# Performance work log

Hardware: AMD Instinct MI355X
Metric: run time of the kernel (lower is better)

## Reference

```python
import jax, jax.numpy as jnp
import numpy as np

N_NODES = 100000


def _gcn_layer(h, W, b, src, dst, norm, n):
    # h: [N, Fin] -> transform then normalized scatter-add aggregation
    h = h @ W                                   # [N, Fout]
    msg = h[src] * norm[:, None]                # [E', Fout] gather + scale
    out = jax.ops.segment_sum(msg, dst, num_segments=n)  # scatter-add
    return out + b


def setup_inputs() -> dict:
    key = jax.random.key(0)
    k1, k2, k3, k4 = jax.random.split(key, 4)
    N, F_IN, HID, C, E = N_NODES, 512, 128, 40, 1600000
    x = jax.random.normal(k1, (N, F_IN), dtype=jnp.float32)
    edge_index = jax.random.randint(k2, (2, E), 0, N, dtype=jnp.int64)
    W1 = jax.random.normal(k3, (F_IN, HID), dtype=jnp.float32) * (1.0 / np.sqrt(F_IN))
    b1 = jnp.zeros((HID,), dtype=jnp.float32)
    W2 = jax.random.normal(k4, (HID, C), dtype=jnp.float32) * (1.0 / np.sqrt(HID))
    b2 = jnp.zeros((C,), dtype=jnp.float32)
    return {"x": x, "edge_index": edge_index, "W1": W1, "b1": b1, "W2": W2, "b2": b2}


def reference(x, edge_index, W1, b1, W2, b2):
    n = x.shape[0]
    # add self-loops (GCNConv default)
    loop = jnp.arange(n, dtype=edge_index.dtype)
    src = jnp.concatenate([edge_index[0], loop])
    dst = jnp.concatenate([edge_index[1], loop])
    # symmetric normalization: deg counted on destination (in-degree, incl. self-loop)
    deg = jax.ops.segment_sum(jnp.ones_like(dst, dtype=x.dtype), dst, num_segments=n)
    dis = jnp.where(deg > 0, jax.lax.rsqrt(deg), 0.0)  # deg^{-1/2}
    norm = dis[src] * dis[dst]                          # per-edge weight

    h = jax.nn.relu(_gcn_layer(x, W1, b1, src, dst, norm, n))
    # dropout: identity in eval mode (training=False)
    h = _gcn_layer(h, W2, b2, src, dst, norm, n)
    return jax.nn.log_softmax(h, axis=1)
```

## Files before the change

### kernel.cpp

```cpp
#include <hip/hip_runtime.h>
#include <hip/hip_bf16.h>


#define F_IN 512
#define HID  128
#define NC   40
#define NCP  48

typedef __attribute__((ext_vector_type(8))) short bf16x8;
typedef __attribute__((ext_vector_type(4))) float f32x4v;

__device__ __forceinline__ ushort f2bf(float f) {
    unsigned r;
    asm("v_cvt_pk_bf16_f32 %0, %1, %1" : "=v"(r) : "v"(f));
    return (ushort)r;
}
__device__ __forceinline__ unsigned cvtpk(float a, float b) {
    unsigned r;
    asm("v_cvt_pk_bf16_f32 %0, %1, %2" : "=v"(r) : "v"(a), "v"(b));
    return r;
}
__device__ __forceinline__ float bf2f(ushort u) {
    return __uint_as_float((unsigned)u << 16);
}
__device__ __forceinline__ bf16x8 cvt8(float4 lo, float4 hi) {
    union { unsigned u[4]; bf16x8 v; } t;
    t.u[0] = cvtpk(lo.x, lo.y); t.u[1] = cvtpk(lo.z, lo.w);
    t.u[2] = cvtpk(hi.x, hi.y); t.u[3] = cvtpk(hi.z, hi.w);
    return t.v;
}

__global__ void prep_k(const int* __restrict__ dst, int E, int EB,
                       unsigned* __restrict__ cnt, int* __restrict__ rank,
                       const float* __restrict__ W1, const float* __restrict__ W2,
                       ushort* __restrict__ W1p, ushort* __restrict__ W2p) {
    int b = blockIdx.x;
    if (b < EB) {
        int t = b * 256 + threadIdx.x;
        if (t < E) rank[t] = (int)atomicAdd(&cnt[dst[t]], 1u);
        return;
    }
    int t = (b - EB) * 256 + threadIdx.x;
    if (t < 65536) {
        int j = t & 7, n = (t >> 3) & 127, kb = (t >> 10) & 3, s = t >> 12;
        int k = s * 32 + kb * 8 + j;
        W1p[t] = f2bf(W1[(size_t)k * HID + n]);
    } else {
        int q = t - 65536;
        if (q < 6144) {
            int j = q & 7;
            int i2 = q >> 3;
            int n = i2 % 48;
            int i3 = i2 / 48;
            int kb = i3 & 3, ks = i3 >> 2;
            int k = ks * 32 + kb * 8 + j;
            float v = (n < NC) ? W2[(size_t)k * NC + n] : 0.f;
            W2p[q] = f2bf(v);
        }
    }
}

__global__ __launch_bounds__(1024) void scan_block(const unsigned* __restrict__ cnt,
                                                   unsigned* __restrict__ offs,
                                                   unsigned* __restrict__ bsums,
                                                   float* __restrict__ dis, int N) {
    int tid = threadIdx.x;
    int i = blockIdx.x * 1024 + tid;
    unsigned v = (i < N) ? cnt[i] : 0u;
    if (i < N) dis[i] = rsqrtf((float)v + 1.0f);
    int lane = tid & 63, w = tid >> 6;
    unsigned s = v;
    #pragma unroll
    for (int d = 1; d < 64; d <<= 1) {
        unsigned t = __shfl_up(s, d, 64);
        if (lane >= d) s += t;
    }
    __shared__ unsigned wt[16];
    if (lane == 63) wt[w] = s;
    __syncthreads();
    unsigned add = 0;
    #pragma unroll
    for (int j = 0; j < 16; j++) add += (j < w) ? wt[j] : 0u;
    unsigned incl = s + add;
    if (i < N) offs[i] = incl - v;
    if (tid == 1023) bsums[blockIdx.x] = incl;
}

__global__ __launch_bounds__(1024) void scan_add2(unsigned* __restrict__ offs,
                                                  const unsigned* __restrict__ bsums,
                                                  int N, unsigned total) {
    int i = blockIdx.x * 1024 + threadIdx.x;
    int lane = threadIdx.x & 63;
    unsigned s = 0;
    for (int j = lane; j < (int)blockIdx.x; j += 64) s += bsums[j];
    #pragma unroll
    for (int d = 1; d < 64; d <<= 1) s += __shfl_xor(s, d, 64);
    if (i < N) offs[i] += s;
    if (i == 0) offs[N] = total;
}

__global__ __launch_bounds__(1024, 4) void fillg1(
        const int* __restrict__ src, const int* __restrict__ dst,
        const unsigned* __restrict__ offs, const int* __restrict__ rank,
        int* __restrict__ col, int E, int F,
        const float* __restrict__ A, const ushort* __restrict__ Bp,
        const float* __restrict__ dis, ushort* __restrict__ C, int N) {
    __shared__ ushort Bs[32768];
    const int bid = blockIdx.x;
    const int tid = threadIdx.x;
    if (bid % 3 == 2) {
        const int stride = F * 1024;
        for (int e = (bid / 3) * 1024 + tid; e < E; e += stride) {
            int d = dst[e];
            col[offs[d] + (unsigned)rank[e]] = src[e];
        }
        return;
    }
    const int g    = bid - bid / 3;
    const int wave = tid >> 6;
    const int lane = tid & 63;
    const int quad = lane >> 4;
    const int mr   = lane & 15;
    const int base = g * 256 + wave * 16;
    const int r0 = base + mr;
    const float* ap0 = A + (size_t)(r0 < N ? r0 : 0) * F_IN + quad * 8;
    const ushort* lbp = Bs + quad * 1024 + mr * 8;

    {
        const uint4* bsrc = (const uint4*)Bp;
        uint4* bdst = (uint4*)Bs;
        #pragma unroll
        for (int r = 0; r < 4; r++) bdst[tid + r * 1024] = bsrc[tid + r * 1024];
    }

    f32x4v acc0[8];
    #pragma unroll
    for (int t = 0; t < 8; t++) acc0[t] = (f32x4v){0.f, 0.f, 0.f, 0.f};

    float4 av[4][2];
    #pragma unroll
    for (int b = 0; b < 4; b++) {
        av[b][0] = *(const float4*)(ap0 + b * 32);
        av[b][1] = *(const float4*)(ap0 + b * 32 + 4);
    }
    __syncthreads();

    #pragma unroll
    for (int s = 0; s < 8; s++) {
        bf16x8 fa = cvt8(av[s & 3][0], av[s & 3][1]);
        av[s & 3][0] = *(const float4*)(ap0 + (s + 4) * 32);
        av[s & 3][1] = *(const float4*)(ap0 + (s + 4) * 32 + 4);
        const ushort* bs = lbp + s * 4096;
        #pragma unroll
        for (int t = 0; t < 8; t++) {
            bf16x8 bb = *(const bf16x8*)(bs + t * 128);
            acc0[t] = __builtin_amdgcn_mfma_f32_16x16x32_bf16(fa, bb, acc0[t], 0, 0, 0);
        }
    }
    __syncthreads();
    {
        const uint4* bsrc = (const uint4*)Bp;
        uint4* bdst = (uint4*)Bs;
        #pragma unroll
        for (int r = 0; r < 4; r++) bdst[tid + r * 1024] = bsrc[4096 + tid + r * 1024];
    }
    __syncthreads();

    #pragma unroll
    for (int s = 8; s < 16; s++) {
        bf16x8 fa = cvt8(av[s & 3][0], av[s & 3][1]);
        if (s < 12) {
            av[s & 3][0] = *(const float4*)(ap0 + (s + 4) * 32);
            av[s & 3][1] = *(const float4*)(ap0 + (s + 4) * 32 + 4);
        }
        const ushort* bs = lbp + (s - 8) * 4096;
        #pragma unroll
        for (int t = 0; t < 8; t++) {
            bf16x8 bb = *(const bf16x8*)(bs + t * 128);
            acc0[t] = __builtin_amdgcn_mfma_f32_16x16x32_bf16(fa, bb, acc0[t], 0, 0, 0);
        }
    }

    #pragma unroll
    for (int rr = 0; rr < 4; rr++) {
        int ra = base + quad * 4 + rr;
        if (ra < N) {
            float ds = dis[ra];
            #pragma unroll
            for (int t = 0; t < 8; t++)
                C[(size_t)ra * HID + t * 16 + mr] = f2bf(acc0[t][rr] * ds);
        }
    }
}

__global__ __launch_bounds__(256) void agg1_k(const ushort* __restrict__ h,
                                              const int* __restrict__ col,
                                              const unsigned* __restrict__ offs,
                                              const float* __restrict__ dis,
                                              const float* __restrict__ b1,
                                              ushort* __restrict__ out, int N) {
    int node = blockIdx.x * 4 + (threadIdx.x >> 6);
    if (node >= N) return;
    int lane = threadIdx.x & 63;
    int ni = lane >> 4;
    int fl = lane & 15;
    const ushort* hb = h + (size_t)fl * 8;
    float a[8] = {0.f, 0.f, 0.f, 0.f, 0.f, 0.f, 0.f, 0.f};
    if (ni == 0) {
        uint4 v = *(const uint4*)(hb + (size_t)node * HID);
        const ushort* u = (const ushort*)&v;
        #pragma unroll
        for (int j = 0; j < 8; j++) a[j] = bf2f(u[j]);
    }
    unsigned p0 = offs[node], p1 = offs[node + 1];
    int s0, s1, s2, s3;
    float w0, w1, w2, w3;
    #define GETC1(pos, sv, wv) { unsigned q_ = (pos); bool v_ = q_ < p1; \
        sv = v_ ? col[q_] : 0; wv = v_ ? 1.f : 0.f; }
    GETC1(p0 + ni,      s0, w0);
    GETC1(p0 + ni + 4,  s1, w1);
    GETC1(p0 + ni + 8,  s2, w2);
    GETC1(p0 + ni + 12, s3, w3);
    for (unsigned p = p0; p < p1; p += 16) {
        int n0, n1, n2, n3;
        float x0, x1, x2, x3;
        GETC1(p + 16 + ni, n0, x0);
        GETC1(p + 20 + ni, n1, x1);
        GETC1(p + 24 + ni, n2, x2);
        GETC1(p + 28 + ni, n3, x3);
        uint4 v0 = *(const uint4*)(hb + (size_t)s0 * HID);
        uint4 v1 = *(const uint4*)(hb + (size_t)s1 * HID);
        uint4 v2 = *(const uint4*)(hb + (size_t)s2 * HID);
        uint4 v3 = *(const uint4*)(hb + (size_t)s3 * HID);
        const ushort* u0 = (const ushort*)&v0;
        const ushort* u1 = (const ushort*)&v1;
        const ushort* u2 = (const ushort*)&v2;
        const ushort* u3 = (const ushort*)&v3;
        #pragma unroll
        for (int j = 0; j < 8; j++)
            a[j] += (w0 * bf2f(u0[j]) + w1 * bf2f(u1[j]))
                  + (w2 * bf2f(u2[j]) + w3 * bf2f(u3[j]));
        s0 = n0; w0 = x0; s1 = n1; w1 = x1;
        s2 = n2; w2 = x2; s3 = n3; w3 = x3;
    }
    #pragma unroll
    for (int j = 0; j < 8; j++) {
        a[j] += __shfl_xor(a[j], 16);
        a[j] += __shfl_xor(a[j], 32);
    }
    if (ni == 0) {
        float dd = dis[node];
        float4 bb0 = *(const float4*)(b1 + fl * 8);
        float4 bb1 = *(const float4*)(b1 + fl * 8 + 4);
        const float bb[8] = {bb0.x, bb0.y, bb0.z, bb0.w, bb1.x, bb1.y, bb1.z, bb1.w};
        __align__(16) ushort o[8];
        #pragma unroll
        for (int j = 0; j < 8; j++) o[j] = f2bf(fmaxf(a[j] * dd + bb[j], 0.f));
        *(uint4*)(out + (size_t)node * HID + (size_t)fl * 8) = *(const uint4*)o;
    }
}

__global__ __launch_bounds__(256) void gemm2_mfma(const ushort* __restrict__ A,
                                                  const ushort* __restrict__ W2p,
                                                  const float* __restrict__ dis,
                                                  ushort* __restrict__ h2, int N) {
    __shared__ ushort Ws[6144];
    const int tid  = threadIdx.x;
    {
        const uint4* s = (const uint4*)W2p;
        uint4* d = (uint4*)Ws;
        #pragma unroll
        for (int r = 0; r < 3; r++) d[tid + r * 256] = s[tid + r * 256];
    }
    __syncthreads();
    const int wave = tid >> 6;
    const int lane = tid & 63;
    const int quad = lane >> 4;
    const int mr   = lane & 15;
    const int base = (blockIdx.x * 4 + wave) * 32;
    if (base >= N) return;
    const int r0 = base + mr;
    const int r1 = base + 16 + mr;
    const bool ok0 = r0 < N, ok1 = r1 < N;
    const ushort* ap0 = A + (size_t)(ok0 ? r0 : 0) * HID + quad * 8;
    const ushort* ap1 = A + (size_t)(ok1 ? r1 : 0) * HID + quad * 8;
    const ushort* bp = Ws + quad * 384 + mr * 8;

    f32x4v acc0[3], acc1[3];
    #pragma unroll
    for (int t = 0; t < 3; t++) {
        acc0[t] = (f32x4v){0.f, 0.f, 0.f, 0.f};
        acc1[t] = (f32x4v){0.f, 0.f, 0.f, 0.f};
    }
    #pragma unroll
    for (int ks = 0; ks < 4; ks++) {
        bf16x8 a0 = *(const bf16x8*)(ap0 + ks * 32);
        bf16x8 a1 = *(const bf16x8*)(ap1 + ks * 32);
        #pragma unroll
        for (int t = 0; t < 3; t++) {
            bf16x8 b = *(const bf16x8*)(bp + ks * 1536 + t * 128);
            acc0[t] = __builtin_amdgcn_mfma_f32_16x16x32_bf16(a0, b, acc0[t], 0, 0, 0);
            acc1[t] = __builtin_amdgcn_mfma_f32_16x16x32_bf16(a1, b, acc1[t], 0, 0, 0);
        }
    }
    #pragma unroll
    for (int rr = 0; rr < 4; rr++) {
        int ra = base + quad * 4 + rr;
        if (ra < N) {
            float ds = dis[ra];
            #pragma unroll
            for (int t = 0; t < 3; t++) {
                int c = t * 16 + mr;
                if (c < NC) h2[(size_t)ra * NCP + c] = f2bf(acc0[t][rr] * ds);
            }
        }
        int rb = base + 16 + quad * 4 + rr;
        if (rb < N) {
            float ds = dis[rb];
            #pragma unroll
            for (int t = 0; t < 3; t++) {
                int c = t * 16 + mr;
                if (c < NC) h2[(size_t)rb * NCP + c] = f2bf(acc1[t][rr] * ds);
            }
        }
    }
}

__global__ __launch_bounds__(256) void agg2_ls(const ushort* __restrict__ h2,
                                               const int* __restrict__ col,
                                               const unsigned* __restrict__ offs,
                                               const float* __restrict__ dis,
                                               const float* __restrict__ b2,
                                               float* __restrict__ out, int N) {
    int node = blockIdx.x * 4 + (threadIdx.x >> 6);
    if (node >= N) return;
    int lane = threadIdx.x & 63;
    int ni = lane >> 3;
    int fl = lane & 7;
    const bool act = fl < 5;
    const ushort* hb = h2 + (size_t)fl * 8;
    float a[8] = {0.f, 0.f, 0.f, 0.f, 0.f, 0.f, 0.f, 0.f};
    if (ni == 0 && act) {
        uint4 v = *(const uint4*)(hb + (size_t)node * NCP);
        const ushort* u = (const ushort*)&v;
        #pragma unroll
        for (int j = 0; j < 8; j++) a[j] = bf2f(u[j]);
    }
    unsigned p0 = offs[node], p1 = offs[node + 1];
    int s0, s1, s2, s3;
    float w0, w1, w2, w3;
    GETC1(p0 + ni,      s0, w0);
    GETC1(p0 + ni + 8,  s1, w1);
    GETC1(p0 + ni + 16, s2, w2);
    GETC1(p0 + ni + 24, s3, w3);
    for (unsigned p = p0; p < p1; p += 32) {
        int n0, n1, n2, n3;
        float x0, x1, x2, x3;
        GETC1(p + 32 + ni, n0, x0);
        GETC1(p + 40 + ni, n1, x1);
        GETC1(p + 48 + ni, n2, x2);
        GETC1(p + 56 + ni, n3, x3);
        if (act) {
            uint4 v0 = *(const uint4*)(hb + (size_t)s0 * NCP);
            uint4 v1 = *(const uint4*)(hb + (size_t)s1 * NCP);
            uint4 v2 = *(const uint4*)(hb + (size_t)s2 * NCP);
            uint4 v3 = *(const uint4*)(hb + (size_t)s3 * NCP);
            const ushort* u0 = (const ushort*)&v0;
            const ushort* u1 = (const ushort*)&v1;
            const ushort* u2 = (const ushort*)&v2;
            const ushort* u3 = (const ushort*)&v3;
            #pragma unroll
            for (int j = 0; j < 8; j++)
                a[j] += (w0 * bf2f(u0[j]) + w1 * bf2f(u1[j]))
                      + (w2 * bf2f(u2[j]) + w3 * bf2f(u3[j]));
        }
        s0 = n0; w0 = x0; s1 = n1; w1 = x1;
        s2 = n2; w2 = x2; s3 = n3; w3 = x3;
    }
    #pragma unroll
    for (int j = 0; j < 8; j++) {
        a[j] += __shfl_xor(a[j], 8);
        a[j] += __shfl_xor(a[j], 16);
        a[j] += __shfl_xor(a[j], 32);
    }
    float dd = dis[node];
    float l[8];
    float m = -1e30f;
    if (act) {
        #pragma unroll
        for (int j = 0; j < 8; j++) {
            l[j] = a[j] * dd + b2[fl * 8 + j];
            m = fmaxf(m, l[j]);
        }
    }
    #pragma unroll
    for (int d = 1; d < 8; d <<= 1) m = fmaxf(m, __shfl_xor(m, d, 8));
    float s = 0.f;
    if (act) {
        #pragma unroll
        for (int j = 0; j < 8; j++) s += __expf(l[j] - m);
    }
    #pragma unroll
    for (int d = 1; d < 8; d <<= 1) s += __shfl_xor(s, d, 8);
    float lse = m + __logf(s);
    if (ni == 0 && act) {
        float* op = out + (size_t)node * NC + fl * 8;
        *(float4*)op       = make_float4(l[0]-lse, l[1]-lse, l[2]-lse, l[3]-lse);
        *(float4*)(op + 4) = make_float4(l[4]-lse, l[5]-lse, l[6]-lse, l[7]-lse);
    }
}

extern "C" void kernel_launch(void* const* d_in, const int* in_sizes, int n_in,
                              void* d_out, int out_size, void* d_ws, size_t ws_size,
                              hipStream_t stream) {
    const float* x  = (const float*)d_in[0];
    const int*   ei = (const int*)d_in[1];
    const float* W1 = (const float*)d_in[2];
    const float* b1 = (const float*)d_in[3];
    const float* W2 = (const float*)d_in[4];
    const float* b2 = (const float*)d_in[5];
    float* out = (float*)d_out;

    const int N = in_sizes[0] / F_IN;
    const int E = in_sizes[1] / 2;
    const int* src = ei;
    const int* dst = ei + E;

    char* ws = (char*)d_ws;
    size_t o = 0;
    unsigned* cnt  = (unsigned*)(ws + o); o += (size_t)N * 4;
    float*    dis  = (float*)   (ws + o); o += (size_t)N * 4;
    unsigned* offs = (unsigned*)(ws + o); o += (size_t)(N + 4) * 4;
    unsigned* bsums= (unsigned*)(ws + o); o += 4096;
    int*      rank = (int*)     (ws + o); o += (size_t)E * 4;
    int*      col  = (int*)     (ws + o); o += (size_t)E * 4;
    o = (o + 15) & ~(size_t)15;
    ushort*   W1p  = (ushort*)  (ws + o); o += (size_t)F_IN * HID * 2;
    o = (o + 15) & ~(size_t)15;
    ushort*   W2p  = (ushort*)  (ws + o); o += 6144 * 2;
    o = (o + 15) & ~(size_t)15;
    ushort*   h1   = (ushort*)  (ws + o); o += (size_t)N * HID * 2;
    o = (o + 15) & ~(size_t)15;
    ushort*   ag1  = (ushort*)  (ws + o); o += (size_t)N * HID * 2;
    o = (o + 15) & ~(size_t)15;
    ushort*   h2   = (ushort*)  (ws + o); o += (size_t)N * NCP * 2;

    const int nb = (N + 1023) / 1024;
    const int EB = (E + 255) / 256;
    const int PB = (65536 + 6144 + 255) / 256;
    const int GB = (N + 255) / 256;

    int T = GB + GB / 2;
    while (T - T / 3 < GB) ++T;
    while (T - T / 3 > GB) --T;
    const int F = T / 3;

    hipMemsetAsync(cnt, 0, (size_t)N * 4, stream);
    prep_k<<<EB + PB, 256, 0, stream>>>(dst, E, EB, cnt, rank, W1, W2, W1p, W2p);
    scan_block<<<nb, 1024, 0, stream>>>(cnt, offs, bsums, dis, N);
    scan_add2<<<nb, 1024, 0, stream>>>(offs, bsums, N, (unsigned)E);

    fillg1<<<T, 1024, 0, stream>>>(src, dst, offs, rank, col, E, F,
                                   x, W1p, dis, h1, N);

    agg1_k<<<(N + 3) / 4, 256, 0, stream>>>(h1, col, offs, dis, b1, ag1, N);

    gemm2_mfma<<<(N + 127) / 128, 256, 0, stream>>>(ag1, W2p, dis, h2, N);
    agg2_ls<<<(N + 3) / 4, 256, 0, stream>>>(h2, col, offs, dis, b2, out, N);
}
```

Baseline: 545.7 us.

## Split GEMM1 across degree-count and CSR-fill kernels, precompute per-edge source weights

The first GEMM is split into two row ranges. The first range runs in the same launch as the atomic degree counting, and the rest runs alongside the CSR column fill. Because the GEMM now runs before dis is known, the source-side normalisation moves into a per-edge weight array wgt filled during the CSR build and read by agg1. The separate memset and prep kernel are folded into a vectorised zeroing/weight-packing kernel, and the A-prefetch depth grows from 4 to 6 stages. This adds an extra E-sized float array to write and read, and hardcodes the split point R1=66560 along with fixed helper block counts.

```diff
diff --git a/kernel.cpp b/kernel.cpp
--- a/kernel.cpp
+++ b/kernel.cpp
@@ -30,17 +30,19 @@
     return t.v;
 }
 
-__global__ void prep_k(const int* __restrict__ dst, int E, int EB,
-                       unsigned* __restrict__ cnt, int* __restrict__ rank,
-                       const float* __restrict__ W1, const float* __restrict__ W2,
-                       ushort* __restrict__ W1p, ushort* __restrict__ W2p) {
+__global__ __launch_bounds__(1024) void init_k(unsigned* __restrict__ cnt, int N,
+                                               int ZB,
+                                               const float* __restrict__ W1,
+                                               const float* __restrict__ W2,
+                                               ushort* __restrict__ W1p,
+                                               ushort* __restrict__ W2p) {
     int b = blockIdx.x;
-    if (b < EB) {
-        int t = b * 256 + threadIdx.x;
-        if (t < E) rank[t] = (int)atomicAdd(&cnt[dst[t]], 1u);
+    if (b < ZB) {
+        int i = b * 4096 + threadIdx.x * 4;
+        if (i < N) *(uint4*)(cnt + i) = (uint4){0u, 0u, 0u, 0u};
         return;
     }
-    int t = (b - EB) * 256 + threadIdx.x;
+    int t = (b - ZB) * 1024 + threadIdx.x;
     if (t < 65536) {
         int j = t & 7, n = (t >> 3) & 127, kb = (t >> 10) & 3, s = t >> 12;
         int k = s * 32 + kb * 8 + j;
@@ -60,6 +62,122 @@
     }
 }
 
+__device__ __forceinline__ void gemm1_block(int blockbase, int tid,
+        const float* __restrict__ A, const ushort* __restrict__ Bp,
+        ushort* __restrict__ C, int N) {
+    __shared__ ushort Bs[32768];
+    const int wave = tid >> 6;
+    const int lane = tid & 63;
+    const int quad = lane >> 4;
+    const int mr   = lane & 15;
+    const int base = blockbase + wave * 16;
+    const int r0 = base + mr;
+    const float* ap0 = A + (size_t)(r0 < N ? r0 : 0) * F_IN + quad * 8;
+    const ushort* lbp = Bs + quad * 1024 + mr * 8;
+
+    {
+        const uint4* bsrc = (const uint4*)Bp;
+        uint4* bdst = (uint4*)Bs;
+        #pragma unroll
+        for (int r = 0; r < 4; r++) bdst[tid + r * 1024] = bsrc[tid + r * 1024];
+    }
+
+    f32x4v acc0[8];
+    #pragma unroll
+    for (int t = 0; t < 8; t++) acc0[t] = (f32x4v){0.f, 0.f, 0.f, 0.f};
+
+    float4 av[6][2];
+    #pragma unroll
+    for (int b = 0; b < 6; b++) {
+        av[b][0] = *(const float4*)(ap0 + b * 32);
+        av[b][1] = *(const float4*)(ap0 + b * 32 + 4);
+    }
+    __syncthreads();
+
+    #pragma unroll
+    for (int s = 0; s < 8; s++) {
+        bf16x8 fa = cvt8(av[s % 6][0], av[s % 6][1]);
+        av[s % 6][0] = *(const float4*)(ap0 + (s + 6) * 32);
+        av[s % 6][1] = *(const float4*)(ap0 + (s + 6) * 32 + 4);
+        const ushort* bs = lbp + s * 4096;
+        #pragma unroll
+        for (int t = 0; t < 8; t++) {
+            bf16x8 bb = *(const bf16x8*)(bs + t * 128);
+            acc0[t] = __builtin_amdgcn_mfma_f32_16x16x32_bf16(fa, bb, acc0[t], 0, 0, 0);
+        }
+    }
+    __syncthreads();
+    {
+        const uint4* bsrc = (const uint4*)Bp;
+        uint4* bdst = (uint4*)Bs;
+        #pragma unroll
+        for (int r = 0; r < 4; r++) bdst[tid + r * 1024] = bsrc[4096 + tid + r * 1024];
+    }
+    __syncthreads();
+
+    #pragma unroll
+    for (int s = 8; s < 16; s++) {
+        bf16x8 fa = cvt8(av[s % 6][0], av[s % 6][1]);
+        if (s < 10) {
+            av[s % 6][0] = *(const float4*)(ap0 + (s + 6) * 32);
+            av[s % 6][1] = *(const float4*)(ap0 + (s + 6) * 32 + 4);
+        }
+        const ushort* bs = lbp + (s - 8) * 4096;
+        #pragma unroll
+        for (int t = 0; t < 8; t++) {
+            bf16x8 bb = *(const bf16x8*)(bs + t * 128);
+            acc0[t] = __builtin_amdgcn_mfma_f32_16x16x32_bf16(fa, bb, acc0[t], 0, 0, 0);
+        }
+    }
+
+    #pragma unroll
+    for (int rr = 0; rr < 4; rr++) {
+        int ra = base + quad * 4 + rr;
+        if (ra < N) {
+            #pragma unroll
+            for (int t = 0; t < 8; t++)
+                C[(size_t)ra * HID + t * 16 + mr] = f2bf(acc0[t][rr]);
+        }
+    }
+}
+
+__global__ __launch_bounds__(1024, 4) void g1prep(
+        const int* __restrict__ dst, int E, int GB1,
+        unsigned* __restrict__ cnt, int* __restrict__ rank,
+        const float* __restrict__ A, const ushort* __restrict__ Bp,
+        ushort* __restrict__ C, int N) {
+    if (blockIdx.x >= GB1) {
+        int t = (blockIdx.x - GB1) * 1024 + threadIdx.x;
+        int stride = ((int)gridDim.x - GB1) * 1024;
+        for (int e = t; e < E; e += stride)
+            rank[e] = (int)atomicAdd(&cnt[dst[e]], 1u);
+        return;
+    }
+    gemm1_block(blockIdx.x * 256, threadIdx.x, A, Bp, C, N);
+}
+
+__global__ __launch_bounds__(1024, 4) void fillg1b(
+        const int* __restrict__ src, const int* __restrict__ dst,
+        const unsigned* __restrict__ offs, const int* __restrict__ rank,
+        const float* __restrict__ dis,
+        int* __restrict__ col, float* __restrict__ wgt, int E, int GB2, int R1,
+        const float* __restrict__ A, const ushort* __restrict__ Bp,
+        ushort* __restrict__ C, int N) {
+    if (blockIdx.x >= GB2) {
+        int t = (blockIdx.x - GB2) * 1024 + threadIdx.x;
+        int stride = ((int)gridDim.x - GB2) * 1024;
+        for (int e = t; e < E; e += stride) {
+            int d = dst[e];
+            int s = src[e];
+            unsigned pos = offs[d] + (unsigned)rank[e];
+            col[pos] = s;
+            wgt[pos] = dis[s];
+        }
+        return;
+    }
+    gemm1_block(R1 + blockIdx.x * 256, threadIdx.x, A, Bp, C, N);
+}
+
 __global__ __launch_bounds__(1024) void scan_block(const unsigned* __restrict__ cnt,
                                                    unsigned* __restrict__ offs,
                                                    unsigned* __restrict__ bsums,
@@ -99,102 +217,9 @@
     if (i == 0) offs[N] = total;
 }
 
-__global__ __launch_bounds__(1024, 4) void fillg1(
-        const int* __restrict__ src, const int* __restrict__ dst,
-        const unsigned* __restrict__ offs, const int* __restrict__ rank,
-        int* __restrict__ col, int E, int F,
-        const float* __restrict__ A, const ushort* __restrict__ Bp,
-        const float* __restrict__ dis, ushort* __restrict__ C, int N) {
-    __shared__ ushort Bs[32768];
-    const int bid = blockIdx.x;
-    const int tid = threadIdx.x;
-    if (bid % 3 == 2) {
-        const int stride = F * 1024;
-        for (int e = (bid / 3) * 1024 + tid; e < E; e += stride) {
-            int d = dst[e];
-            col[offs[d] + (unsigned)rank[e]] = src[e];
-        }
-        return;
-    }
-    const int g    = bid - bid / 3;
-    const int wave = tid >> 6;
-    const int lane = tid & 63;
-    const int quad = lane >> 4;
-    const int mr   = lane & 15;
-    const int base = g * 256 + wave * 16;
-    const int r0 = base + mr;
-    const float* ap0 = A + (size_t)(r0 < N ? r0 : 0) * F_IN + quad * 8;
-    const ushort* lbp = Bs + quad * 1024 + mr * 8;
-
-    {
-        const uint4* bsrc = (const uint4*)Bp;
-        uint4* bdst = (uint4*)Bs;
-        #pragma unroll
-        for (int r = 0; r < 4; r++) bdst[tid + r * 1024] = bsrc[tid + r * 1024];
-    }
-
-    f32x4v acc0[8];
-    #pragma unroll
-    for (int t = 0; t < 8; t++) acc0[t] = (f32x4v){0.f, 0.f, 0.f, 0.f};
-
-    float4 av[4][2];
-    #pragma unroll
-    for (int b = 0; b < 4; b++) {
-        av[b][0] = *(const float4*)(ap0 + b * 32);
-        av[b][1] = *(const float4*)(ap0 + b * 32 + 4);
-    }
-    __syncthreads();
-
-    #pragma unroll
-    for (int s = 0; s < 8; s++) {
-        bf16x8 fa = cvt8(av[s & 3][0], av[s & 3][1]);
-        av[s & 3][0] = *(const float4*)(ap0 + (s + 4) * 32);
-        av[s & 3][1] = *(const float4*)(ap0 + (s + 4) * 32 + 4);
-        const ushort* bs = lbp + s * 4096;
-        #pragma unroll
-        for (int t = 0; t < 8; t++) {
-            bf16x8 bb = *(const bf16x8*)(bs + t * 128);
-            acc0[t] = __builtin_amdgcn_mfma_f32_16x16x32_bf16(fa, bb, acc0[t], 0, 0, 0);
-        }
-    }
-    __syncthreads();
-    {
-        const uint4* bsrc = (const uint4*)Bp;
-        uint4* bdst = (uint4*)Bs;
-        #pragma unroll
-        for (int r = 0; r < 4; r++) bdst[tid + r * 1024] = bsrc[4096 + tid + r * 1024];
-    }
-    __syncthreads();
-
-    #pragma unroll
-    for (int s = 8; s < 16; s++) {
-        bf16x8 fa = cvt8(av[s & 3][0], av[s & 3][1]);
-        if (s < 12) {
-            av[s & 3][0] = *(const float4*)(ap0 + (s + 4) * 32);
-            av[s & 3][1] = *(const float4*)(ap0 + (s + 4) * 32 + 4);
-        }
-        const ushort* bs = lbp + (s - 8) * 4096;
-        #pragma unroll
-        for (int t = 0; t < 8; t++) {
-            bf16x8 bb = *(const bf16x8*)(bs + t * 128);
-            acc0[t] = __builtin_amdgcn_mfma_f32_16x16x32_bf16(fa, bb, acc0[t], 0, 0, 0);
-        }
-    }
-
-    #pragma unroll
-    for (int rr = 0; rr < 4; rr++) {
-        int ra = base + quad * 4 + rr;
-        if (ra < N) {
-            float ds = dis[ra];
-            #pragma unroll
-            for (int t = 0; t < 8; t++)
-                C[(size_t)ra * HID + t * 16 + mr] = f2bf(acc0[t][rr] * ds);
-        }
-    }
-}
-
 __global__ __launch_bounds__(256) void agg1_k(const ushort* __restrict__ h,
                                               const int* __restrict__ col,
+                                              const float* __restrict__ wgt,
                                               const unsigned* __restrict__ offs,
                                               const float* __restrict__ dis,
                                               const float* __restrict__ b1,
@@ -205,29 +230,30 @@
     int ni = lane >> 4;
     int fl = lane & 15;
     const ushort* hb = h + (size_t)fl * 8;
+    float dd = dis[node];
     float a[8] = {0.f, 0.f, 0.f, 0.f, 0.f, 0.f, 0.f, 0.f};
     if (ni == 0) {
         uint4 v = *(const uint4*)(hb + (size_t)node * HID);
         const ushort* u = (const ushort*)&v;
         #pragma unroll
-        for (int j = 0; j < 8; j++) a[j] = bf2f(u[j]);
+        for (int j = 0; j < 8; j++) a[j] = dd * bf2f(u[j]);
     }
     unsigned p0 = offs[node], p1 = offs[node + 1];
     int s0, s1, s2, s3;
     float w0, w1, w2, w3;
-    #define GETC1(pos, sv, wv) { unsigned q_ = (pos); bool v_ = q_ < p1; \
-        sv = v_ ? col[q_] : 0; wv = v_ ? 1.f : 0.f; }
-    GETC1(p0 + ni,      s0, w0);
-    GETC1(p0 + ni + 4,  s1, w1);
-    GETC1(p0 + ni + 8,  s2, w2);
-    GETC1(p0 + ni + 12, s3, w3);
+    #define GETW(pos, sv, wv) { unsigned q_ = (pos); bool v_ = q_ < p1; \
+        sv = v_ ? col[q_] : 0; wv = v_ ? wgt[q_] : 0.f; }
+    GETW(p0 + ni,      s0, w0);
+    GETW(p0 + ni + 4,  s1, w1);
+    GETW(p0 + ni + 8,  s2, w2);
+    GETW(p0 + ni + 12, s3, w3);
     for (unsigned p = p0; p < p1; p += 16) {
         int n0, n1, n2, n3;
         float x0, x1, x2, x3;
-        GETC1(p + 16 + ni, n0, x0);
-        GETC1(p + 20 + ni, n1, x1);
-        GETC1(p + 24 + ni, n2, x2);
-        GETC1(p + 28 + ni, n3, x3);
+        GETW(p + 16 + ni, n0, x0);
+        GETW(p + 20 + ni, n1, x1);
+        GETW(p + 24 + ni, n2, x2);
+        GETW(p + 28 + ni, n3, x3);
         uint4 v0 = *(const uint4*)(hb + (size_t)s0 * HID);
         uint4 v1 = *(const uint4*)(hb + (size_t)s1 * HID);
         uint4 v2 = *(const uint4*)(hb + (size_t)s2 * HID);
@@ -249,7 +275,6 @@
         a[j] += __shfl_xor(a[j], 32);
     }
     if (ni == 0) {
-        float dd = dis[node];
         float4 bb0 = *(const float4*)(b1 + fl * 8);
         float4 bb1 = *(const float4*)(b1 + fl * 8 + 4);
         const float bb[8] = {bb0.x, bb0.y, bb0.z, bb0.w, bb1.x, bb1.y, bb1.z, bb1.w};
@@ -349,6 +374,8 @@
     unsigned p0 = offs[node], p1 = offs[node + 1];
     int s0, s1, s2, s3;
     float w0, w1, w2, w3;
+    #define GETC1(pos, sv, wv) { unsigned q_ = (pos); bool v_ = q_ < p1; \
+        sv = v_ ? col[q_] : 0; wv = v_ ? 1.f : 0.f; }
     GETC1(p0 + ni,      s0, w0);
     GETC1(p0 + ni + 8,  s1, w1);
     GETC1(p0 + ni + 16, s2, w2);
@@ -434,6 +461,7 @@
     unsigned* bsums= (unsigned*)(ws + o); o += 4096;
     int*      rank = (int*)     (ws + o); o += (size_t)E * 4;
     int*      col  = (int*)     (ws + o); o += (size_t)E * 4;
+    float*    wgt  = (float*)   (ws + o); o += (size_t)E * 4;
     o = (o + 15) & ~(size_t)15;
     ushort*   W1p  = (ushort*)  (ws + o); o += (size_t)F_IN * HID * 2;
     o = (o + 15) & ~(size_t)15;
@@ -446,24 +474,28 @@
     ushort*   h2   = (ushort*)  (ws + o); o += (size_t)N * NCP * 2;
 
     const int nb = (N + 1023) / 1024;
-    const int EB = (E + 255) / 256;
-    const int PB = (65536 + 6144 + 255) / 256;
-    const int GB = (N + 255) / 256;
-
-    int T = GB + GB / 2;
-    while (T - T / 3 < GB) ++T;
-    while (T - T / 3 > GB) --T;
-    const int F = T / 3;
-
-    hipMemsetAsync(cnt, 0, (size_t)N * 4, stream);
-    prep_k<<<EB + PB, 256, 0, stream>>>(dst, E, EB, cnt, rank, W1, W2, W1p, W2p);
+    const int ZB = (N + 4095) / 4096;
+    const int PWB = (65536 + 6144 + 1023) / 1024;
+
+    const int R1  = 66560;
+    const int GB1 = R1 / 256;
+    const int GB2 = (N - R1 + 255) / 256;
+    const int PREPB = 384;
+    const int FB    = 192;
+
+    init_k<<<ZB + PWB, 1024, 0, stream>>>(cnt, N, ZB, W1, W2, W1p, W2p);
+
+    g1prep<<<GB1 + PREPB, 1024, 0, stream>>>(dst, E, GB1, cnt, rank,
+                                             x, W1p, h1, N);
+
     scan_block<<<nb, 1024, 0, stream>>>(cnt, offs, bsums, dis, N);
     scan_add2<<<nb, 1024, 0, stream>>>(offs, bsums, N, (unsigned)E);
 
-    fillg1<<<T, 1024, 0, stream>>>(src, dst, offs, rank, col, E, F,
-                                   x, W1p, dis, h1, N);
-
-    agg1_k<<<(N + 3) / 4, 256, 0, stream>>>(h1, col, offs, dis, b1, ag1, N);
+    fillg1b<<<GB2 + FB, 1024, 0, stream>>>(src, dst, offs, rank, dis,
+                                           col, wgt, E, GB2, R1,
+                                           x, W1p, h1, N);
+
+    agg1_k<<<(N + 3) / 4, 256, 0, stream>>>(h1, col, wgt, offs, dis, b1, ag1, N);
 
     gemm2_mfma<<<(N + 127) / 128, 256, 0, stream>>>(ag1, W2p, dis, h2, N);
     agg2_ls<<<(N + 3) / 4, 256, 0, stream>>>(h2, col, offs, dis, b2, out, N);
```

Measured after the change: 602.3 us. +10.4%, slower.
